# Performance work log

Measured on AMD Instinct MI355X. Metric: run time of the kernel, lower is better.

Reference implementation:

```python
import math
import jax, jax.numpy as jnp
import numpy as np

H = 8
D = 32  # c_hidden per head


def setup_inputs() -> dict:
    key = jax.random.key(0)
    ks = jax.random.split(key, 10)
    B, Q, K, C = 2, 2048, 2048, 256
    s = 1.0 / math.sqrt(C)
    return {
        "q_x": jax.random.normal(ks[0], (B, Q, C), jnp.float32),
        "kv_x": jax.random.normal(ks[1], (B, K, C), jnp.float32),
        "bias_mask": jax.random.normal(ks[2], (B, 1, 1, K), jnp.float32),
        "bias_pair": jax.random.normal(ks[3], (1, H, Q, K), jnp.float32),
        "Wq": jax.random.normal(ks[4], (H * D, C), jnp.float32) * s,
        "Wk": jax.random.normal(ks[5], (H * D, C), jnp.float32) * s,
        "Wv": jax.random.normal(ks[6], (H * D, C), jnp.float32) * s,
        "Wo": jax.random.normal(ks[7], (C, H * D), jnp.float32) * s,
        "bo": jnp.zeros((C,), jnp.float32),
        "Wg": jax.random.normal(ks[8], (H * D, C), jnp.float32) * s,
        "bg": jnp.zeros((H * D,), jnp.float32),
    }


def reference(q_x, kv_x, bias_mask, bias_pair, Wq, Wk, Wv, Wo, bo, Wg, bg):
    B, Q, C = q_x.shape
    K = kv_x.shape[-2]
    # projections (torch Linear: x @ W.T), split heads -> [B,H,L,D]
    q = (q_x @ Wq.T).reshape(B, Q, H, D).swapaxes(-2, -3) / math.sqrt(D)
    k = (kv_x @ Wk.T).reshape(B, K, H, D).swapaxes(-2, -3)
    v = (kv_x @ Wv.T).reshape(B, K, H, D).swapaxes(-2, -3)
    scores = jnp.einsum("bhqd,bhkd->bhqk", q, k) + bias_mask + bias_pair
    w = jax.nn.softmax(scores, axis=-1)
    o = jnp.einsum("bhqk,bhkd->bhqd", w, v).swapaxes(-2, -3)  # [B,Q,H,D]
    g = jax.nn.sigmoid(q_x @ Wg.T + bg).reshape(B, Q, H, D)
    o = o * g
    return o.reshape(B, Q, H * D) @ Wo.T + bo
```

## Files before the change

kernel.cpp:

```cpp
#include <hip/hip_runtime.h>
#include <hip/hip_bf16.h>
#include <stdint.h>
#include <math.h>

typedef __attribute__((ext_vector_type(8))) short bf16x8;
typedef __attribute__((ext_vector_type(4))) float f32x4;

#define HQ 2048
#define HK 2048
#define NH 8
#define ND 32
#define NC 256

union U8 { uint32_t u[4]; bf16x8 v; };

__device__ __forceinline__ uint16_t f2bf(float f) {
  uint32_t u = __float_as_uint(f);
  u += 0x7FFFu + ((u >> 16) & 1u);
  return (uint16_t)(u >> 16);
}
__device__ __forceinline__ uint32_t pack2bf(float a, float b) {
  return (uint32_t)f2bf(a) | ((uint32_t)f2bf(b) << 16);
}
__device__ __forceinline__ int swz64(int row, int piece) {
  int s = (((row >> 3) & 1) << 1) | ((row >> 1) & 1);
  return row * 64 + ((piece ^ s) << 4);
}
__device__ __forceinline__ f32x4 mfma32(bf16x8 a, bf16x8 b, f32x4 c) {
  return __builtin_amdgcn_mfma_f32_16x16x32_bf16(a, b, c, 0, 0, 0);
}
__device__ __forceinline__ void dma16(const void* g, void* l) {
  __builtin_amdgcn_global_load_lds(
      (const __attribute__((address_space(1))) uint32_t*)g,
      (__attribute__((address_space(3))) uint32_t*)l, 16, 0, 0);
}

__global__ __launch_bounds__(256) void proj_kernel(
    const float* __restrict__ qx, const float* __restrict__ kvx,
    const float* __restrict__ Wq, const float* __restrict__ Wk,
    const float* __restrict__ Wv, const float* __restrict__ Wg,
    const float* __restrict__ bg,
    uint16_t* __restrict__ q_p, uint16_t* __restrict__ k_p,
    uint16_t* __restrict__ v_p, float* __restrict__ g_ws)
{
  const int bx = blockIdx.x;
  const int Mb = bx & 63, Nb = (bx >> 6) & 3, p = bx >> 8;
  const int Mbase = Mb * 64, Nbase = Nb * 64;
  const float* X = (p == 0 || p == 3) ? qx : kvx;
  const float* W = (p == 0) ? Wq : (p == 1) ? Wk : (p == 2) ? Wv : Wg;

  __shared__ __align__(16) uint16_t smem[4096];
  uint16_t* sX = smem;
  uint16_t* sW = smem + 2048;

  const int tid = threadIdx.x;
  const int l = tid & 63, w = tid >> 6;
  const int qq = l & 15, g = l >> 4;
  const int row = tid >> 2, gp = tid & 3;

  f32x4 acc[4] = {};

  for (int ks = 0; ks < 8; ++ks) {
    const float* xs = X + (size_t)(Mbase + row) * 256 + ks * 32 + gp * 8;
    f32x4 x0 = *(const f32x4*)xs;
    f32x4 x1 = *(const f32x4*)(xs + 4);
    const float* ws_ = W + (size_t)(Nbase + row) * 256 + ks * 32 + gp * 8;
    f32x4 w0 = *(const f32x4*)ws_;
    f32x4 w1 = *(const f32x4*)(ws_ + 4);
    U8 ux, uw;
    ux.u[0] = pack2bf(x0[0], x0[1]); ux.u[1] = pack2bf(x0[2], x0[3]);
    ux.u[2] = pack2bf(x1[0], x1[1]); ux.u[3] = pack2bf(x1[2], x1[3]);
    uw.u[0] = pack2bf(w0[0], w0[1]); uw.u[1] = pack2bf(w0[2], w0[3]);
    uw.u[2] = pack2bf(w1[0], w1[1]); uw.u[3] = pack2bf(w1[2], w1[3]);
    __syncthreads();
    *(bf16x8*)((char*)sX + swz64(row, gp)) = ux.v;
    *(bf16x8*)((char*)sW + swz64(row, gp)) = uw.v;
    __syncthreads();
    bf16x8 a = *(bf16x8*)((char*)sX + swz64(w * 16 + qq, g));
#pragma unroll
    for (int nf = 0; nf < 4; ++nf) {
      bf16x8 bb = *(bf16x8*)((char*)sW + swz64(nf * 16 + qq, g));
      acc[nf] = mfma32(a, bb, acc[nf]);
    }
  }

  if (p == 2) {
    __syncthreads();
#pragma unroll
    for (int nf = 0; nf < 4; ++nf) {
      int n_loc = nf * 16 + qq;
#pragma unroll
      for (int r = 0; r < 4; ++r) {
        int m_loc = w * 16 + 4 * g + r;
        int byte = n_loc * 128 + ((((m_loc >> 3) ^ (n_loc & 7)) << 4)) + (m_loc & 7) * 2;
        *(uint16_t*)((char*)smem + byte) = f2bf(acc[nf][r]);
      }
    }
    __syncthreads();
    const int n_loc = tid >> 2, mp = tid & 3;
    const int ng = Nbase + n_loc;
    const int hh = ng >> 5, dd = ng & 31;
    const int bb_ = Mbase >> 11;
#pragma unroll
    for (int jj = 0; jj < 2; ++jj) {
      int piece = mp * 2 + jj;
      bf16x8 vv = *(bf16x8*)((char*)smem + n_loc * 128 + ((piece ^ (n_loc & 7)) << 4));
      int seq = (Mbase & 2047) + piece * 8;
      *(bf16x8*)(v_p + ((size_t)(bb_ * NH + hh) * ND + dd) * (size_t)HK + seq) = vv;
    }
    return;
  }

#pragma unroll
  for (int nf = 0; nf < 4; ++nf) {
    int n = Nbase + nf * 16 + qq;
#pragma unroll
    for (int r = 0; r < 4; ++r) {
      int m = Mbase + w * 16 + 4 * g + r;
      float val = acc[nf][r];
      if (p == 0) {
        val *= 0.17677669529663687f;
        int bb_ = m >> 11, seq = m & 2047, hh = n >> 5, dd = n & 31;
        q_p[((size_t)(bb_ * NH + hh) * HQ + seq) * ND + dd] = f2bf(val);
      } else if (p == 1) {
        int bb_ = m >> 11, seq = m & 2047, hh = n >> 5, dd = n & 31;
        k_p[((size_t)(bb_ * NH + hh) * HK + seq) * ND + dd] = f2bf(val);
      } else {
        g_ws[(size_t)m * NC + n] = 1.f / (1.f + __expf(-(val + bg[n])));
      }
    }
  }
}

__global__ __launch_bounds__(256, 2) void attn_kernel(
    const uint16_t* __restrict__ q_p, const uint16_t* __restrict__ k_p,
    const uint16_t* __restrict__ v_p, const float* __restrict__ bias_mask,
    const float* __restrict__ bias_pair,
    float* __restrict__ O_ws, float* __restrict__ l_ws)
{
  const int bx = blockIdx.x;
  const int kh = bx & 1, h = (bx >> 1) & 7, qt = bx >> 4;

  __shared__ __align__(16) char LDS[65536];
  char* sK = LDS;
  char* sV = LDS + 16384;
  char* sP = LDS + 32768;

  const int tid = threadIdx.x;
  const int l = tid & 63, wq = tid >> 6;
  const int qq = l & 15, g = l >> 4;
  const int q_glob = qt * 64 + wq * 16 + qq;

  bf16x8 qf0 = *(const bf16x8*)(q_p + ((size_t)h * HQ + q_glob) * ND + g * 8);
  bf16x8 qf1 = *(const bf16x8*)(q_p + ((size_t)(NH + h) * HQ + q_glob) * ND + g * 8);

  int kOffLane;
  {
    int B = wq * 1024 + l * 16;
    int Lr = B >> 7, q8 = l & 7;
    int hp = q8 ^ (Lr & 7);
    int half = hp >> 2, pc = hp & 3;
    int s = Lr * 2 + half, F = s >> 4, qs = s & 15;
    int krow = 8 * (qs >> 2) + (qs & 3) + (F & 1) * 4 + (F >> 1) * 32;
    kOffLane = krow * 64 + pc * 16;
  }
  const char* kSrc0 = (const char*)(k_p + (size_t)h * HK * ND) + kh * 65536 + kOffLane;
  const char* kSrc1 = (const char*)(k_p + (size_t)(NH + h) * HK * ND) + kh * 65536 + kOffLane;
  int vOffLane;
  {
    int B = wq * 1024 + l * 16;
    int d = B >> 7, q8 = l & 7;
    int pc = q8 ^ (d & 7);
    vOffLane = d * (HK * 2) + pc * 16;
  }
  const char* vSrc0 = (const char*)(v_p + (size_t)h * ND * (size_t)HK) + kh * 2048 + vOffLane;
  const char* vSrc1 = (const char*)(v_p + (size_t)(NH + h) * ND * (size_t)HK) + kh * 2048 + vOffLane;
  const char* pSrc0; const char* pSrc1; const char* pSrc2; const char* pSrc3;
  {
    const char* bpBlk = (const char*)bias_pair + ((size_t)h * HQ + qt * 64) * (size_t)HK * 4 + kh * 4096;
    int q16 = l & 15;
#define BP_SRC(jj) ({ int row = (wq * 4 + (jj)) * 4 + (l >> 4); \
                      int pc = (q16 & 8) | ((q16 & 7) ^ (row & 7)); \
                      bpBlk + (size_t)row * HK * 4 + pc * 16; })
    pSrc0 = BP_SRC(0); pSrc1 = BP_SRC(1); pSrc2 = BP_SRC(2); pSrc3 = BP_SRC(3);
#undef BP_SRC
  }

  int afOff[4], vaOff[4], bpOff[4];
#pragma unroll
  for (int F = 0; F < 4; ++F) {
    int Ls = 8 * F + (qq >> 1);
    afOff[F] = Ls * 128 + (((qq & 1) * 4 + g) ^ (qq >> 1)) * 16;
  }
#pragma unroll
  for (int hd = 0; hd < 2; ++hd)
#pragma unroll
    for (int c = 0; c < 2; ++c) {
      int d = hd * 16 + qq;
      vaOff[hd * 2 + c] = d * 128 + ((4 * c + g) ^ (d & 7)) * 16;
    }
#pragma unroll
  for (int F = 0; F < 4; ++F) {
    int piece = 8 * (F >> 1) + 2 * g + (F & 1);
    int row = wq * 16 + qq;
    bpOff[F] = row * 256 + ((piece & 8) | ((piece & 7) ^ (row & 7))) * 16;
  }

#define STAGE(tt, dbi) do { \
    dma16(kSrc0 + (size_t)(tt) * 4096, sK + (dbi) * 8192 + wq * 1024); \
    dma16(kSrc1 + (size_t)(tt) * 4096, sK + (dbi) * 8192 + 4096 + wq * 1024); \
    dma16(vSrc0 + (size_t)(tt) * 128,  sV + (dbi) * 8192 + wq * 1024); \
    dma16(vSrc1 + (size_t)(tt) * 128,  sV + (dbi) * 8192 + 4096 + wq * 1024); \
    dma16(pSrc0 + (size_t)(tt) * 256,  sP + (dbi) * 16384 + wq * 4096); \
    dma16(pSrc1 + (size_t)(tt) * 256,  sP + (dbi) * 16384 + wq * 4096 + 1024); \
    dma16(pSrc2 + (size_t)(tt) * 256,  sP + (dbi) * 16384 + wq * 4096 + 2048); \
    dma16(pSrc3 + (size_t)(tt) * 256,  sP + (dbi) * 16384 + wq * 4096 + 3072); \
  } while (0)

  f32x4 o00 = {}, o01 = {}, o10 = {}, o11 = {};
  float l0 = 0.f, l1 = 0.f;
  const float* bmb0 = bias_mask + kh * 1024;
  const float* bmb1 = bias_mask + HK + kh * 1024;

  STAGE(0, 0);

#pragma unroll 1
  for (int t = 0; t < 16; ++t) {
    const int bi = t & 1;
    if (t < 15) {
      STAGE(t + 1, bi ^ 1);
      asm volatile("s_waitcnt vmcnt(8)" ::: "memory");
    } else {
      asm volatile("s_waitcnt vmcnt(0)" ::: "memory");
    }
    __builtin_amdgcn_s_barrier();
    __builtin_amdgcn_sched_barrier(0);

    const char* bP = sP + bi * 16384;
    f32x4 bp0 = *(const f32x4*)(bP + bpOff[0]);
    f32x4 bp1 = *(const f32x4*)(bP + bpOff[1]);
    f32x4 bp2 = *(const f32x4*)(bP + bpOff[2]);
    f32x4 bp3 = *(const f32x4*)(bP + bpOff[3]);
    const int t64 = t * 64;

    {
      const char* bK = sK + bi * 8192;
      const char* bV = sV + bi * 8192;
      bf16x8 af0 = *(const bf16x8*)(bK + afOff[0]);
      bf16x8 af1 = *(const bf16x8*)(bK + afOff[1]);
      bf16x8 af2 = *(const bf16x8*)(bK + afOff[2]);
      bf16x8 af3 = *(const bf16x8*)(bK + afOff[3]);
      f32x4 z = {};
      f32x4 s0 = mfma32(af0, qf0, z);
      f32x4 s1 = mfma32(af1, qf0, z);
      f32x4 s2 = mfma32(af2, qf0, z);
      f32x4 s3 = mfma32(af3, qf0, z);
      f32x4 bm0 = *(const f32x4*)(bmb0 + t64 + 8 * g);
      f32x4 bm1 = *(const f32x4*)(bmb0 + t64 + 8 * g + 4);
      f32x4 bm2 = *(const f32x4*)(bmb0 + t64 + 32 + 8 * g);
      f32x4 bm3 = *(const f32x4*)(bmb0 + t64 + 32 + 8 * g + 4);
#pragma unroll
      for (int r = 0; r < 4; ++r) {
        s0[r] += bp0[r] + bm0[r];
        s1[r] += bp1[r] + bm1[r];
        s2[r] += bp2[r] + bm2[r];
        s3[r] += bp3[r] + bm3[r];
      }
      uint32_t pbk[4][2];
      {
        float p0 = __expf(s0[0]), p1 = __expf(s0[1]);
        float p2 = __expf(s0[2]), p3 = __expf(s0[3]);
        l0 += (p0 + p1) + (p2 + p3);
        pbk[0][0] = pack2bf(p0, p1); pbk[0][1] = pack2bf(p2, p3);
        p0 = __expf(s1[0]); p1 = __expf(s1[1]);
        p2 = __expf(s1[2]); p3 = __expf(s1[3]);
        l0 += (p0 + p1) + (p2 + p3);
        pbk[1][0] = pack2bf(p0, p1); pbk[1][1] = pack2bf(p2, p3);
        p0 = __expf(s2[0]); p1 = __expf(s2[1]);
        p2 = __expf(s2[2]); p3 = __expf(s2[3]);
        l0 += (p0 + p1) + (p2 + p3);
        pbk[2][0] = pack2bf(p0, p1); pbk[2][1] = pack2bf(p2, p3);
        p0 = __expf(s3[0]); p1 = __expf(s3[1]);
        p2 = __expf(s3[2]); p3 = __expf(s3[3]);
        l0 += (p0 + p1) + (p2 + p3);
        pbk[3][0] = pack2bf(p0, p1); pbk[3][1] = pack2bf(p2, p3);
      }
      U8 bu0, bu1;
      bu0.u[0] = pbk[0][0]; bu0.u[1] = pbk[0][1];
      bu0.u[2] = pbk[1][0]; bu0.u[3] = pbk[1][1];
      bu1.u[0] = pbk[2][0]; bu1.u[1] = pbk[2][1];
      bu1.u[2] = pbk[3][0]; bu1.u[3] = pbk[3][1];
      bf16x8 va00 = *(const bf16x8*)(bV + vaOff[0]);
      bf16x8 va01 = *(const bf16x8*)(bV + vaOff[1]);
      bf16x8 va10 = *(const bf16x8*)(bV + vaOff[2]);
      bf16x8 va11 = *(const bf16x8*)(bV + vaOff[3]);
      o00 = mfma32(va00, bu0.v, o00);
      o01 = mfma32(va10, bu0.v, o01);
      o00 = mfma32(va01, bu1.v, o00);
      o01 = mfma32(va11, bu1.v, o01);
    }
    {
      const char* bK = sK + bi * 8192 + 4096;
      const char* bV = sV + bi * 8192 + 4096;
      bf16x8 af0 = *(const bf16x8*)(bK + afOff[0]);
      bf16x8 af1 = *(const bf16x8*)(bK + afOff[1]);
      bf16x8 af2 = *(const bf16x8*)(bK + afOff[2]);
      bf16x8 af3 = *(const bf16x8*)(bK + afOff[3]);
      f32x4 z = {};
      f32x4 s0 = mfma32(af0, qf1, z);
      f32x4 s1 = mfma32(af1, qf1, z);
      f32x4 s2 = mfma32(af2, qf1, z);
      f32x4 s3 = mfma32(af3, qf1, z);
      f32x4 bm0 = *(const f32x4*)(bmb1 + t64 + 8 * g);
      f32x4 bm1 = *(const f32x4*)(bmb1 + t64 + 8 * g + 4);
      f32x4 bm2 = *(const f32x4*)(bmb1 + t64 + 32 + 8 * g);
      f32x4 bm3 = *(const f32x4*)(bmb1 + t64 + 32 + 8 * g + 4);
#pragma unroll
      for (int r = 0; r < 4; ++r) {
        s0[r] += bp0[r] + bm0[r];
        s1[r] += bp1[r] + bm1[r];
        s2[r] += bp2[r] + bm2[r];
        s3[r] += bp3[r] + bm3[r];
      }
      uint32_t pbk[4][2];
      {
        float p0 = __expf(s0[0]), p1 = __expf(s0[1]);
        float p2 = __expf(s0[2]), p3 = __expf(s0[3]);
        l1 += (p0 + p1) + (p2 + p3);
        pbk[0][0] = pack2bf(p0, p1); pbk[0][1] = pack2bf(p2, p3);
        p0 = __expf(s1[0]); p1 = __expf(s1[1]);
        p2 = __expf(s1[2]); p3 = __expf(s1[3]);
        l1 += (p0 + p1) + (p2 + p3);
        pbk[1][0] = pack2bf(p0, p1); pbk[1][1] = pack2bf(p2, p3);
        p0 = __expf(s2[0]); p1 = __expf(s2[1]);
        p2 = __expf(s2[2]); p3 = __expf(s2[3]);
        l1 += (p0 + p1) + (p2 + p3);
        pbk[2][0] = pack2bf(p0, p1); pbk[2][1] = pack2bf(p2, p3);
        p0 = __expf(s3[0]); p1 = __expf(s3[1]);
        p2 = __expf(s3[2]); p3 = __expf(s3[3]);
        l1 += (p0 + p1) + (p2 + p3);
        pbk[3][0] = pack2bf(p0, p1); pbk[3][1] = pack2bf(p2, p3);
      }
      U8 bu0, bu1;
      bu0.u[0] = pbk[0][0]; bu0.u[1] = pbk[0][1];
      bu0.u[2] = pbk[1][0]; bu0.u[3] = pbk[1][1];
      bu1.u[0] = pbk[2][0]; bu1.u[1] = pbk[2][1];
      bu1.u[2] = pbk[3][0]; bu1.u[3] = pbk[3][1];
      bf16x8 va00 = *(const bf16x8*)(bV + vaOff[0]);
      bf16x8 va01 = *(const bf16x8*)(bV + vaOff[1]);
      bf16x8 va10 = *(const bf16x8*)(bV + vaOff[2]);
      bf16x8 va11 = *(const bf16x8*)(bV + vaOff[3]);
      o10 = mfma32(va00, bu0.v, o10);
      o11 = mfma32(va10, bu0.v, o11);
      o10 = mfma32(va01, bu1.v, o10);
      o11 = mfma32(va11, bu1.v, o11);
    }

    __builtin_amdgcn_sched_barrier(0);
    __builtin_amdgcn_s_barrier();
  }
#undef STAGE

  l0 += __shfl_xor(l0, 16, 64);
  l0 += __shfl_xor(l0, 32, 64);
  l1 += __shfl_xor(l1, 16, 64);
  l1 += __shfl_xor(l1, 32, 64);
#pragma unroll
  for (int b = 0; b < 2; ++b) {
    f32x4 oa = b ? o10 : o00;
    f32x4 ob = b ? o11 : o01;
    float lr = b ? l1 : l0;
    __syncthreads();
    float* se = (float*)LDS + wq * 576;
#pragma unroll
    for (int r = 0; r < 4; ++r) {
      se[qq * 36 + 4 * g + r]      = oa[r];
      se[qq * 36 + 16 + 4 * g + r] = ob[r];
    }
    if (g == 0) l_ws[kh * 32768 + b * 16384 + h * 2048 + q_glob] = lr;
    __syncthreads();
    const int qrow = l >> 2, pc = l & 3;
    const float* sr = (float*)LDS + wq * 576 + qrow * 36 + pc * 8;
    f32x4 x0 = *(const f32x4*)sr;
    f32x4 x1 = *(const f32x4*)(sr + 4);
    const int q_out = qt * 64 + wq * 16 + qrow;
    float* dst = O_ws + ((size_t)((kh * 2 + b) * HQ + q_out)) * NC + h * ND + pc * 8;
    *(f32x4*)dst = x0;
    *(f32x4*)(dst + 4) = x1;
  }
}

__global__ __launch_bounds__(256) void outproj_kernel(
    const float* __restrict__ O_ws, const float* __restrict__ l_ws,
    const float* __restrict__ g_ws, const float* __restrict__ Wo,
    const float* __restrict__ bo, float* __restrict__ out)
{
  const int bx = blockIdx.x;
  const int Mb = bx & 63, Nb = bx >> 6;
  const int Mbase = Mb * 64, Nbase = Nb * 64;
  __shared__ __align__(16) uint16_t smem2[4096];
  uint16_t* sA = smem2;
  uint16_t* sB = smem2 + 2048;
  const int tid = threadIdx.x;
  const int l = tid & 63, w = tid >> 6;
  const int qq = l & 15, g = l >> 4;
  const int row = tid >> 2, gp = tid & 3;
  const int m = Mbase + row, bb2 = m >> 11, qloc = m & 2047;
  f32x4 acc[4] = {};
  for (int ks = 0; ks < 8; ++ks) {
    const size_t lidx = (size_t)bb2 * 16384 + (size_t)ks * 2048 + qloc;
    const float inv = 1.f / (l_ws[lidx] + l_ws[32768 + lidx]);
    const int col = ks * 32 + gp * 8;
    const float* o0p = O_ws + ((size_t)(bb2 * HQ + qloc)) * NC + col;
    const float* o1p = O_ws + ((size_t)((2 + bb2) * HQ + qloc)) * NC + col;
    const float* gpp = g_ws + ((size_t)(bb2 * HQ + qloc)) * NC + col;
    f32x4 a0 = *(const f32x4*)o0p;      f32x4 a1 = *(const f32x4*)(o0p + 4);
    f32x4 b0 = *(const f32x4*)o1p;      f32x4 b1 = *(const f32x4*)(o1p + 4);
    f32x4 g0 = *(const f32x4*)gpp;      f32x4 g1 = *(const f32x4*)(gpp + 4);
#pragma unroll
    for (int r = 0; r < 4; ++r) {
      a0[r] = (a0[r] + b0[r]) * inv * g0[r];
      a1[r] = (a1[r] + b1[r]) * inv * g1[r];
    }
    const float* wsrc = Wo + (size_t)(Nbase + row) * 256 + ks * 32 + gp * 8;
    f32x4 w0 = *(const f32x4*)wsrc;
    f32x4 w1 = *(const f32x4*)(wsrc + 4);
    U8 ua, uw;
    ua.u[0] = pack2bf(a0[0], a0[1]); ua.u[1] = pack2bf(a0[2], a0[3]);
    ua.u[2] = pack2bf(a1[0], a1[1]); ua.u[3] = pack2bf(a1[2], a1[3]);
    uw.u[0] = pack2bf(w0[0], w0[1]); uw.u[1] = pack2bf(w0[2], w0[3]);
    uw.u[2] = pack2bf(w1[0], w1[1]); uw.u[3] = pack2bf(w1[2], w1[3]);
    __syncthreads();
    *(bf16x8*)((char*)sA + swz64(row, gp)) = ua.v;
    *(bf16x8*)((char*)sB + swz64(row, gp)) = uw.v;
    __syncthreads();
    bf16x8 a = *(bf16x8*)((char*)sA + swz64(w * 16 + qq, g));
#pragma unroll
    for (int nf = 0; nf < 4; ++nf) {
      bf16x8 bb = *(bf16x8*)((char*)sB + swz64(nf * 16 + qq, g));
      acc[nf] = mfma32(a, bb, acc[nf]);
    }
  }
#pragma unroll
  for (int nf = 0; nf < 4; ++nf) {
    int n = Nbase + nf * 16 + qq;
    float bias = bo[n];
#pragma unroll
    for (int r = 0; r < 4; ++r) {
      int mm = Mbase + w * 16 + 4 * g + r;
      out[(size_t)mm * NC + n] = acc[nf][r] + bias;
    }
  }
}

extern "C" void kernel_launch(void* const* d_in, const int* in_sizes, int n_in,
                              void* d_out, int out_size, void* d_ws, size_t ws_size,
                              hipStream_t stream) {
  (void)in_sizes; (void)n_in; (void)out_size; (void)ws_size;
  const float* qx        = (const float*)d_in[0];
  const float* kvx       = (const float*)d_in[1];
  const float* bias_mask = (const float*)d_in[2];
  const float* bias_pair = (const float*)d_in[3];
  const float* Wq        = (const float*)d_in[4];
  const float* Wk        = (const float*)d_in[5];
  const float* Wv        = (const float*)d_in[6];
  const float* Wo        = (const float*)d_in[7];
  const float* bo        = (const float*)d_in[8];
  const float* Wg        = (const float*)d_in[9];
  const float* bg        = (const float*)d_in[10];

  char* ws = (char*)d_ws;
  uint16_t* q_p  = (uint16_t*)(ws);
  uint16_t* k_p  = (uint16_t*)(ws + (2u << 20));
  uint16_t* v_p  = (uint16_t*)(ws + (4u << 20));
  float*    g_ws = (float*)   (ws + (6u << 20));
  float*    O_ws = (float*)   (ws + (10u << 20));
  float*    l_ws = (float*)   (ws + (18u << 20));
  float* out = (float*)d_out;

  proj_kernel<<<dim3(1024), dim3(256), 0, stream>>>(qx, kvx, Wq, Wk, Wv, Wg, bg,
                                                    q_p, k_p, v_p, g_ws);
  attn_kernel<<<dim3(512), dim3(256), 0, stream>>>(q_p, k_p, v_p, bias_mask,
                                                   bias_pair, O_ws, l_ws);
  outproj_kernel<<<dim3(256), dim3(256), 0, stream>>>(O_ws, l_ws, g_ws, Wo, bo, out);
}
```

Before: 65.09 us.

## Split attention keys four ways with 512-thread blocks sharing bias_pair tiles

The attention kernel now uses 512-thread blocks covering 128 query rows, with the key range split four ways instead of two. Each K/V stage is loaded by the half of the waves matching a batch, rather than every wave loading both batches. The bias_pair buffer is now single-buffered: it is read into registers, a barrier follows, and only then is the next stage prefetched, which frees LDS but waits on all loads every iteration. The output projection now sums four partial O and l results, which adds workspace traffic, and launch bounds (512,4) may put pressure on registers.

```diff
diff --git a/kernel.cpp b/kernel.cpp
--- a/kernel.cpp
+++ b/kernel.cpp
@@ -132,14 +132,14 @@
   }
 }
 
-__global__ __launch_bounds__(256, 2) void attn_kernel(
+__global__ __launch_bounds__(512, 4) void attn_kernel(
     const uint16_t* __restrict__ q_p, const uint16_t* __restrict__ k_p,
     const uint16_t* __restrict__ v_p, const float* __restrict__ bias_mask,
     const float* __restrict__ bias_pair,
     float* __restrict__ O_ws, float* __restrict__ l_ws)
 {
   const int bx = blockIdx.x;
-  const int kh = bx & 1, h = (bx >> 1) & 7, qt = bx >> 4;
+  const int khq = bx & 3, h = (bx >> 2) & 7, qt = bx >> 5;
 
   __shared__ __align__(16) char LDS[65536];
   char* sK = LDS;
@@ -149,14 +149,15 @@
   const int tid = threadIdx.x;
   const int l = tid & 63, wq = tid >> 6;
   const int qq = l & 15, g = l >> 4;
-  const int q_glob = qt * 64 + wq * 16 + qq;
+  const int ws4 = wq & 3, bsel = wq >> 2;
+  const int q_glob = qt * 128 + wq * 16 + qq;
 
   bf16x8 qf0 = *(const bf16x8*)(q_p + ((size_t)h * HQ + q_glob) * ND + g * 8);
   bf16x8 qf1 = *(const bf16x8*)(q_p + ((size_t)(NH + h) * HQ + q_glob) * ND + g * 8);
 
   int kOffLane;
   {
-    int B = wq * 1024 + l * 16;
+    int B = ws4 * 1024 + l * 16;
     int Lr = B >> 7, q8 = l & 7;
     int hp = q8 ^ (Lr & 7);
     int half = hp >> 2, pc = hp & 3;
@@ -164,24 +165,25 @@
     int krow = 8 * (qs >> 2) + (qs & 3) + (F & 1) * 4 + (F >> 1) * 32;
     kOffLane = krow * 64 + pc * 16;
   }
-  const char* kSrc0 = (const char*)(k_p + (size_t)h * HK * ND) + kh * 65536 + kOffLane;
-  const char* kSrc1 = (const char*)(k_p + (size_t)(NH + h) * HK * ND) + kh * 65536 + kOffLane;
+  const char* kSrcB = (const char*)(k_p + (size_t)(bsel * NH + h) * HK * ND)
+                      + khq * 32768 + kOffLane;
   int vOffLane;
   {
-    int B = wq * 1024 + l * 16;
+    int B = ws4 * 1024 + l * 16;
     int d = B >> 7, q8 = l & 7;
     int pc = q8 ^ (d & 7);
     vOffLane = d * (HK * 2) + pc * 16;
   }
-  const char* vSrc0 = (const char*)(v_p + (size_t)h * ND * (size_t)HK) + kh * 2048 + vOffLane;
-  const char* vSrc1 = (const char*)(v_p + (size_t)(NH + h) * ND * (size_t)HK) + kh * 2048 + vOffLane;
+  const char* vSrcB = (const char*)(v_p + (size_t)(bsel * NH + h) * ND * (size_t)HK)
+                      + khq * 1024 + vOffLane;
   const char* pSrc0; const char* pSrc1; const char* pSrc2; const char* pSrc3;
   {
-    const char* bpBlk = (const char*)bias_pair + ((size_t)h * HQ + qt * 64) * (size_t)HK * 4 + kh * 4096;
+    const char* bpBlk = (const char*)bias_pair
+        + ((size_t)h * HQ + qt * 128) * (size_t)HK * 4 + khq * 2048;
     int q16 = l & 15;
-#define BP_SRC(jj) ({ int row = (wq * 4 + (jj)) * 4 + (l >> 4); \
+#define BP_SRC(jj) ({ int row = wq * 16 + (jj) * 4 + (l >> 4); \
                       int pc = (q16 & 8) | ((q16 & 7) ^ (row & 7)); \
-                      bpBlk + (size_t)row * HK * 4 + pc * 16; })
+                      bpBlk + (size_t)row * (HK * 4) + pc * 16; })
     pSrc0 = BP_SRC(0); pSrc1 = BP_SRC(1); pSrc2 = BP_SRC(2); pSrc3 = BP_SRC(3);
 #undef BP_SRC
   }
@@ -207,42 +209,39 @@
   }
 
 #define STAGE(tt, dbi) do { \
-    dma16(kSrc0 + (size_t)(tt) * 4096, sK + (dbi) * 8192 + wq * 1024); \
-    dma16(kSrc1 + (size_t)(tt) * 4096, sK + (dbi) * 8192 + 4096 + wq * 1024); \
-    dma16(vSrc0 + (size_t)(tt) * 128,  sV + (dbi) * 8192 + wq * 1024); \
-    dma16(vSrc1 + (size_t)(tt) * 128,  sV + (dbi) * 8192 + 4096 + wq * 1024); \
-    dma16(pSrc0 + (size_t)(tt) * 256,  sP + (dbi) * 16384 + wq * 4096); \
-    dma16(pSrc1 + (size_t)(tt) * 256,  sP + (dbi) * 16384 + wq * 4096 + 1024); \
-    dma16(pSrc2 + (size_t)(tt) * 256,  sP + (dbi) * 16384 + wq * 4096 + 2048); \
-    dma16(pSrc3 + (size_t)(tt) * 256,  sP + (dbi) * 16384 + wq * 4096 + 3072); \
+    dma16(kSrcB + (size_t)(tt) * 4096, sK + (dbi) * 8192 + bsel * 4096 + ws4 * 1024); \
+    dma16(vSrcB + (size_t)(tt) * 128,  sV + (dbi) * 8192 + bsel * 4096 + ws4 * 1024); \
+    dma16(pSrc0 + (size_t)(tt) * 256,  sP + wq * 4096); \
+    dma16(pSrc1 + (size_t)(tt) * 256,  sP + wq * 4096 + 1024); \
+    dma16(pSrc2 + (size_t)(tt) * 256,  sP + wq * 4096 + 2048); \
+    dma16(pSrc3 + (size_t)(tt) * 256,  sP + wq * 4096 + 3072); \
   } while (0)
 
   f32x4 o00 = {}, o01 = {}, o10 = {}, o11 = {};
   float l0 = 0.f, l1 = 0.f;
-  const float* bmb0 = bias_mask + kh * 1024;
-  const float* bmb1 = bias_mask + HK + kh * 1024;
+  const float* bmb0 = bias_mask + khq * 512;
+  const float* bmb1 = bias_mask + HK + khq * 512;
 
   STAGE(0, 0);
 
 #pragma unroll 1
-  for (int t = 0; t < 16; ++t) {
+  for (int t = 0; t < 8; ++t) {
     const int bi = t & 1;
-    if (t < 15) {
-      STAGE(t + 1, bi ^ 1);
-      asm volatile("s_waitcnt vmcnt(8)" ::: "memory");
-    } else {
-      asm volatile("s_waitcnt vmcnt(0)" ::: "memory");
-    }
+    asm volatile("s_waitcnt vmcnt(0)" ::: "memory");
     __builtin_amdgcn_s_barrier();
     __builtin_amdgcn_sched_barrier(0);
 
-    const char* bP = sP + bi * 16384;
-    f32x4 bp0 = *(const f32x4*)(bP + bpOff[0]);
-    f32x4 bp1 = *(const f32x4*)(bP + bpOff[1]);
-    f32x4 bp2 = *(const f32x4*)(bP + bpOff[2]);
-    f32x4 bp3 = *(const f32x4*)(bP + bpOff[3]);
+    f32x4 bp0 = *(const f32x4*)(sP + bpOff[0]);
+    f32x4 bp1 = *(const f32x4*)(sP + bpOff[1]);
+    f32x4 bp2 = *(const f32x4*)(sP + bpOff[2]);
+    f32x4 bp3 = *(const f32x4*)(sP + bpOff[3]);
+    asm volatile("s_waitcnt lgkmcnt(0)" ::: "memory");
+    __builtin_amdgcn_sched_barrier(0);
+    __builtin_amdgcn_s_barrier();
+
+    if (t < 7) STAGE(t + 1, bi ^ 1);
+
     const int t64 = t * 64;
-
     {
       const char* bK = sK + bi * 8192;
       const char* bV = sV + bi * 8192;
@@ -355,9 +354,6 @@
       o10 = mfma32(va01, bu1.v, o10);
       o11 = mfma32(va11, bu1.v, o11);
     }
-
-    __builtin_amdgcn_sched_barrier(0);
-    __builtin_amdgcn_s_barrier();
   }
 #undef STAGE
 
@@ -377,14 +373,14 @@
       se[qq * 36 + 4 * g + r]      = oa[r];
       se[qq * 36 + 16 + 4 * g + r] = ob[r];
     }
-    if (g == 0) l_ws[kh * 32768 + b * 16384 + h * 2048 + q_glob] = lr;
+    if (g == 0) l_ws[khq * 32768 + b * 16384 + h * 2048 + q_glob] = lr;
     __syncthreads();
     const int qrow = l >> 2, pc = l & 3;
     const float* sr = (float*)LDS + wq * 576 + qrow * 36 + pc * 8;
     f32x4 x0 = *(const f32x4*)sr;
     f32x4 x1 = *(const f32x4*)(sr + 4);
-    const int q_out = qt * 64 + wq * 16 + qrow;
-    float* dst = O_ws + ((size_t)((kh * 2 + b) * HQ + q_out)) * NC + h * ND + pc * 8;
+    const int q_out = qt * 128 + wq * 16 + qrow;
+    float* dst = O_ws + ((size_t)((khq * 2 + b) * HQ + q_out)) * NC + h * ND + pc * 8;
     *(f32x4*)dst = x0;
     *(f32x4*)(dst + 4) = x1;
   }
@@ -408,19 +404,25 @@
   const int m = Mbase + row, bb2 = m >> 11, qloc = m & 2047;
   f32x4 acc[4] = {};
   for (int ks = 0; ks < 8; ++ks) {
-    const size_t lidx = (size_t)bb2 * 16384 + (size_t)ks * 2048 + qloc;
-    const float inv = 1.f / (l_ws[lidx] + l_ws[32768 + lidx]);
+    const size_t lbase = (size_t)bb2 * 16384 + (size_t)ks * 2048 + qloc;
+    const float inv = 1.f / (l_ws[lbase] + l_ws[32768 + lbase] +
+                             l_ws[65536 + lbase] + l_ws[98304 + lbase]);
     const int col = ks * 32 + gp * 8;
-    const float* o0p = O_ws + ((size_t)(bb2 * HQ + qloc)) * NC + col;
-    const float* o1p = O_ws + ((size_t)((2 + bb2) * HQ + qloc)) * NC + col;
+    f32x4 a0 = {}, a1 = {};
+#pragma unroll
+    for (int kq = 0; kq < 4; ++kq) {
+      const float* op = O_ws + ((size_t)((kq * 2 + bb2) * HQ + qloc)) * NC + col;
+      f32x4 t0 = *(const f32x4*)op;
+      f32x4 t1 = *(const f32x4*)(op + 4);
+#pragma unroll
+      for (int r = 0; r < 4; ++r) { a0[r] += t0[r]; a1[r] += t1[r]; }
+    }
     const float* gpp = g_ws + ((size_t)(bb2 * HQ + qloc)) * NC + col;
-    f32x4 a0 = *(const f32x4*)o0p;      f32x4 a1 = *(const f32x4*)(o0p + 4);
-    f32x4 b0 = *(const f32x4*)o1p;      f32x4 b1 = *(const f32x4*)(o1p + 4);
     f32x4 g0 = *(const f32x4*)gpp;      f32x4 g1 = *(const f32x4*)(gpp + 4);
 #pragma unroll
     for (int r = 0; r < 4; ++r) {
-      a0[r] = (a0[r] + b0[r]) * inv * g0[r];
-      a1[r] = (a1[r] + b1[r]) * inv * g1[r];
+      a0[r] = a0[r] * inv * g0[r];
+      a1[r] = a1[r] * inv * g1[r];
     }
     const float* wsrc = Wo + (size_t)(Nbase + row) * 256 + ks * 32 + gp * 8;
     f32x4 w0 = *(const f32x4*)wsrc;
@@ -475,12 +477,12 @@
   uint16_t* v_p  = (uint16_t*)(ws + (4u << 20));
   float*    g_ws = (float*)   (ws + (6u << 20));
   float*    O_ws = (float*)   (ws + (10u << 20));
-  float*    l_ws = (float*)   (ws + (18u << 20));
+  float*    l_ws = (float*)   (ws + (26u << 20));
   float* out = (float*)d_out;
 
   proj_kernel<<<dim3(1024), dim3(256), 0, stream>>>(qx, kvx, Wq, Wk, Wv, Wg, bg,
                                                     q_p, k_p, v_p, g_ws);
-  attn_kernel<<<dim3(512), dim3(256), 0, stream>>>(q_p, k_p, v_p, bias_mask,
+  attn_kernel<<<dim3(512), dim3(512), 0, stream>>>(q_p, k_p, v_p, bias_mask,
                                                    bias_pair, O_ws, l_ws);
   outproj_kernel<<<dim3(256), dim3(256), 0, stream>>>(O_ws, l_ws, g_ws, Wo, bo, out);
 }
```

After: 69.12 us. +6.2%, slower.
